# Optimization experiments

Hardware: AMD Instinct MI355X
Metric: run time of the kernel (lower is better)

Reference implementation:

```python
import jax, jax.numpy as jnp
import numpy as np

B, S, D = 2, 2048, 640
H, DH = 8, 80  # heads, dim_head
SCALE = DH ** -0.5


def setup_inputs() -> dict:
    key = jax.random.key(0)
    ks = jax.random.split(key, 7)
    std = D ** -0.5
    return {
        "x": jax.random.normal(ks[0], (B, S, D), jnp.float32),
        "encoder_hidden_states": jax.random.normal(ks[1], (B, S, D), jnp.float32),
        # Linear weights stored as [in, out] so application is x @ W
        "Wq": jax.random.normal(ks[2], (D, H * DH), jnp.float32) * std,
        "Wk": jax.random.normal(ks[3], (D, H * DH), jnp.float32) * std,
        "Wv": jax.random.normal(ks[4], (D, H * DH), jnp.float32) * std,
        "Wo": jax.random.normal(ks[5], (H * DH, D), jnp.float32) * std,
        "bo": jax.random.normal(ks[6], (D,), jnp.float32) * 0.01,
    }


def reference(x, encoder_hidden_states, Wq, Wk, Wv, Wo, bo):
    # projections (to_q/to_k/to_v have bias=False)
    q = x @ Wq                      # [B, S, H*DH]
    k = encoder_hidden_states @ Wk  # [B, S, H*DH]
    v = encoder_hidden_states @ Wv  # [B, S, H*DH]

    def split_heads(t):
        b, s, _ = t.shape
        return t.reshape(b, s, H, DH).transpose(0, 2, 1, 3)  # [B, H, S, DH]

    q, k, v = split_heads(q), split_heads(k), split_heads(v)

    # the torch loop over bh-chunks computes plain softmax attention; same math fused
    scores = jnp.einsum("bhid,bhjd->bhij", q, k) * SCALE  # [B, H, Sq, Skv]
    attn = jax.nn.softmax(scores, axis=-1)
    out = jnp.einsum("bhij,bhjd->bhid", attn, v)          # [B, H, Sq, DH]

    out = out.transpose(0, 2, 1, 3).reshape(x.shape[0], x.shape[1], H * DH)
    return out @ Wo + bo  # to_out[0]; Dropout(p=0) is identity
```

## Files before the change

### kernel.cpp

```cpp
#include <hip/hip_runtime.h>
#include <hip/hip_bf16.h>

typedef __bf16 v4bf __attribute__((ext_vector_type(4)));
typedef __bf16 v8bf __attribute__((ext_vector_type(8)));
typedef float  v4f  __attribute__((ext_vector_type(4)));

namespace {
constexpr int Bb  = 2;
constexpr int Ss  = 2048;
constexpr int Dd  = 640;
constexpr int Hh  = 8;
constexpr int DHh = 80;
constexpr int Mm  = Bb * Ss;
constexpr float kQScale = 0.11180339887498949f * 1.4426950408889634f;

__device__ __forceinline__ float4 ld4(const float* p) {
  return *reinterpret_cast<const float4*>(p);
}
}

__global__ __launch_bounds__(256)
void wtrans_kernel(const float* __restrict__ Wq, const float* __restrict__ Wk,
                   const float* __restrict__ Wv, const float* __restrict__ Wo,
                   __bf16* __restrict__ Wtq, __bf16* __restrict__ Wtk,
                   __bf16* __restrict__ Wtv, __bf16* __restrict__ Wto) {
  const int z = blockIdx.z;
  const float* W = (z == 0) ? Wq : (z == 1) ? Wk : (z == 2) ? Wv : Wo;
  __bf16* Wt = (z == 0) ? Wtq : (z == 1) ? Wtk : (z == 2) ? Wtv : Wto;
  const int k0 = blockIdx.y * 32, n0 = blockIdx.x * 32;
  __shared__ float t[32][33];
  const int tid = threadIdx.x;
  {
    int kr = tid >> 3, c4 = (tid & 7) * 4;
    float4 f = ld4(W + (size_t)(k0 + kr) * Dd + n0 + c4);
    t[kr][c4 + 0] = f.x; t[kr][c4 + 1] = f.y;
    t[kr][c4 + 2] = f.z; t[kr][c4 + 3] = f.w;
  }
  __syncthreads();
  {
    int nr = tid >> 3, kc = (tid & 7) * 4;
    v4bf p;
#pragma unroll
    for (int u = 0; u < 4; ++u) p[u] = (__bf16)t[kc + u][nr];
    *reinterpret_cast<v4bf*>(&Wt[(size_t)(n0 + nr) * Dd + k0 + kc]) = p;
  }
}

template <bool AF32>
__device__ __forceinline__ void gemm_core_db(const void* __restrict__ Ap,
                                             const __bf16* __restrict__ Bt,
                                             __bf16* As, __bf16* Bs, int m0,
                                             int n0, int rh, int ch,
                                             v4f acc[4][4]) {
  constexpr int BUF = 128 * 40;
  constexpr int NKB = Dd / 32;
  const int tid = threadIdx.x;
  const int lane = tid & 63;
  const int quad = lane >> 4, l15 = lane & 15;
  const int lr = tid >> 1;
  const int lk = (tid & 1) * 16;
  const __bf16* Bg = Bt + (size_t)(n0 + lr) * Dd + lk;
  const float* Af = (const float*)Ap;
  const __bf16* Ab = (const __bf16*)Ap;

#pragma unroll
  for (int i = 0; i < 4; ++i)
#pragma unroll
    for (int j = 0; j < 4; ++j) acc[i][j] = (v4f){0.f, 0.f, 0.f, 0.f};

  v8bf a0, a1, b0, b1;
  if constexpr (AF32) {
    const float* ap = Af + (size_t)(m0 + lr) * Dd + lk;
    float4 f0 = ld4(ap), f1 = ld4(ap + 4), f2 = ld4(ap + 8), f3 = ld4(ap + 12);
    a0[0]=(__bf16)f0.x; a0[1]=(__bf16)f0.y; a0[2]=(__bf16)f0.z; a0[3]=(__bf16)f0.w;
    a0[4]=(__bf16)f1.x; a0[5]=(__bf16)f1.y; a0[6]=(__bf16)f1.z; a0[7]=(__bf16)f1.w;
    a1[0]=(__bf16)f2.x; a1[1]=(__bf16)f2.y; a1[2]=(__bf16)f2.z; a1[3]=(__bf16)f2.w;
    a1[4]=(__bf16)f3.x; a1[5]=(__bf16)f3.y; a1[6]=(__bf16)f3.z; a1[7]=(__bf16)f3.w;
  } else {
    const __bf16* ap = Ab + (size_t)(m0 + lr) * Dd + lk;
    a0 = *reinterpret_cast<const v8bf*>(ap);
    a1 = *reinterpret_cast<const v8bf*>(ap + 8);
  }
  b0 = *reinterpret_cast<const v8bf*>(Bg);
  b1 = *reinterpret_cast<const v8bf*>(Bg + 8);
  *reinterpret_cast<v8bf*>(&As[lr * 40 + lk])     = a0;
  *reinterpret_cast<v8bf*>(&As[lr * 40 + lk + 8]) = a1;
  *reinterpret_cast<v8bf*>(&Bs[lr * 40 + lk])     = b0;
  *reinterpret_cast<v8bf*>(&Bs[lr * 40 + lk + 8]) = b1;

  for (int it = 0; it < NKB; ++it) {
    if (it + 1 < NKB) {
      const int kb = (it + 1) * 32;
      if constexpr (AF32) {
        const float* ap = Af + (size_t)(m0 + lr) * Dd + kb + lk;
        float4 f0 = ld4(ap), f1 = ld4(ap + 4), f2 = ld4(ap + 8),
               f3 = ld4(ap + 12);
        a0[0]=(__bf16)f0.x; a0[1]=(__bf16)f0.y; a0[2]=(__bf16)f0.z; a0[3]=(__bf16)f0.w;
        a0[4]=(__bf16)f1.x; a0[5]=(__bf16)f1.y; a0[6]=(__bf16)f1.z; a0[7]=(__bf16)f1.w;
        a1[0]=(__bf16)f2.x; a1[1]=(__bf16)f2.y; a1[2]=(__bf16)f2.z; a1[3]=(__bf16)f2.w;
        a1[4]=(__bf16)f3.x; a1[5]=(__bf16)f3.y; a1[6]=(__bf16)f3.z; a1[7]=(__bf16)f3.w;
      } else {
        const __bf16* ap = Ab + (size_t)(m0 + lr) * Dd + kb + lk;
        a0 = *reinterpret_cast<const v8bf*>(ap);
        a1 = *reinterpret_cast<const v8bf*>(ap + 8);
      }
      b0 = *reinterpret_cast<const v8bf*>(Bg + kb);
      b1 = *reinterpret_cast<const v8bf*>(Bg + kb + 8);
    }
    __syncthreads();
    const int cur = (it & 1) * BUF, nxt = BUF - cur;
    v8bf af[4], bv[4];
#pragma unroll
    for (int i = 0; i < 4; ++i)
      af[i] = *reinterpret_cast<const v8bf*>(
          &As[cur + (rh + i * 16 + l15) * 40 + quad * 8]);
#pragma unroll
    for (int j = 0; j < 4; ++j)
      bv[j] = *reinterpret_cast<const v8bf*>(
          &Bs[cur + (ch + j * 16 + l15) * 40 + quad * 8]);
#pragma unroll
    for (int i = 0; i < 4; ++i)
#pragma unroll
      for (int j = 0; j < 4; ++j)
        acc[i][j] = __builtin_amdgcn_mfma_f32_16x16x32_bf16(af[i], bv[j],
                                                            acc[i][j], 0, 0, 0);
    if (it + 1 < NKB) {
      *reinterpret_cast<v8bf*>(&As[nxt + lr * 40 + lk])     = a0;
      *reinterpret_cast<v8bf*>(&As[nxt + lr * 40 + lk + 8]) = a1;
      *reinterpret_cast<v8bf*>(&Bs[nxt + lr * 40 + lk])     = b0;
      *reinterpret_cast<v8bf*>(&Bs[nxt + lr * 40 + lk + 8]) = b1;
    }
  }
}

__global__ __launch_bounds__(256)
void gemm_qkv_mfma(const float* __restrict__ x, const float* __restrict__ ehs,
                   const __bf16* __restrict__ Wtq,
                   const __bf16* __restrict__ Wtk,
                   const __bf16* __restrict__ Wtv, __bf16* __restrict__ qb,
                   __bf16* __restrict__ kbuf, __bf16* __restrict__ vb) {
  const int z = blockIdx.z;
  const float* A = (z == 0) ? x : ehs;
  const __bf16* Bt = (z == 0) ? Wtq : (z == 1) ? Wtk : Wtv;
  __bf16* C = (z == 0) ? qb : (z == 1) ? kbuf : vb;
  const float scale = (z == 0) ? kQScale : 1.0f;

  __shared__ __bf16 As[2 * 128 * 40];
  __shared__ __bf16 Bs[2 * 128 * 40];
  const int tid = threadIdx.x;
  const int w = tid >> 6, lane = tid & 63;
  const int quad = lane >> 4, l15 = lane & 15;
  const int m0 = blockIdx.y * 128, n0 = blockIdx.x * 128;
  const int rh = (w >> 1) * 64, ch = (w & 1) * 64;
  v4f acc[4][4];
  gemm_core_db<true>(A, Bt, As, Bs, m0, n0, rh, ch, acc);

  if (z == 2) {
#pragma unroll
    for (int i = 0; i < 4; ++i)
#pragma unroll
      for (int j = 0; j < 4; ++j) {
        int m = m0 + rh + i * 16 + quad * 4;
        int n = n0 + ch + j * 16 + l15;
        int bb = m >> 11, tok = m & 2047;
        v4bf pk;
#pragma unroll
        for (int r = 0; r < 4; ++r) pk[r] = (__bf16)acc[i][j][r];
        *reinterpret_cast<v4bf*>(&C[((size_t)bb * Dd + n) * Ss + tok]) = pk;
      }
  } else {
#pragma unroll
    for (int i = 0; i < 4; ++i)
#pragma unroll
      for (int j = 0; j < 4; ++j) {
        int m = m0 + rh + i * 16 + quad * 4;
        int n = n0 + ch + j * 16 + l15;
#pragma unroll
        for (int r = 0; r < 4; ++r)
          C[(size_t)(m + r) * Dd + n] = (__bf16)(acc[i][j][r] * scale);
      }
  }
}

__global__ __launch_bounds__(256)
void gemm_out_mfma(const __bf16* __restrict__ A, const __bf16* __restrict__ Bt,
                   const float* __restrict__ bias, float* __restrict__ out) {
  __shared__ __bf16 As[2 * 128 * 40];
  __shared__ __bf16 Bs[2 * 128 * 40];
  const int tid = threadIdx.x;
  const int w = tid >> 6, lane = tid & 63;
  const int quad = lane >> 4, l15 = lane & 15;
  const int m0 = blockIdx.y * 128, n0 = blockIdx.x * 128;
  const int rh = (w >> 1) * 64, ch = (w & 1) * 64;
  v4f acc[4][4];
  gemm_core_db<false>(A, Bt, As, Bs, m0, n0, rh, ch, acc);

#pragma unroll
  for (int i = 0; i < 4; ++i)
#pragma unroll
    for (int j = 0; j < 4; ++j) {
      int m = m0 + rh + i * 16 + quad * 4;
      int n = n0 + ch + j * 16 + l15;
      float bn = bias[n];
#pragma unroll
      for (int r = 0; r < 4; ++r)
        out[(size_t)(m + r) * Dd + n] = acc[i][j][r] + bn;
    }
}

__global__ __launch_bounds__(256, 2)
void attn_mfma_kernel(const __bf16* __restrict__ q,
                      const __bf16* __restrict__ k,
                      const __bf16* __restrict__ vtg, __bf16* __restrict__ o) {
  constexpr int QT = 64;
  constexpr int KT = 32;
  constexpr int KW = Ss / 4;
  constexpr int NIT = KW / KT;
  constexpr int LQ = 104;
  constexpr int LV = 40;
  constexpr int KS = KT * LQ;
  constexpr int VS = 96 * LV;
  constexpr int PS = QT * LV;
  constexpr int WSZ = KS + VS + PS;
  constexpr int LM = 100;

  __shared__ __align__(16) __bf16 smem[4 * WSZ];

  const int bh = blockIdx.y;
  const int b = bh >> 3, h = bh & 7;
  const int q0 = blockIdx.x * QT;
  const int tid = threadIdx.x;
  const int w = tid >> 6;
  const int lane = tid & 63;
  const int quad = lane >> 4;
  const int l15 = lane & 15;

  __bf16* ksw = smem + w * WSZ;
  __bf16* vtw = ksw + KS;
  __bf16* psw = vtw + VS;

  const __bf16* qg  = q + (size_t)(b * Ss + q0) * Dd + h * DHh;
  const __bf16* kgb = k + (size_t)(b * Ss) * Dd + h * DHh;
  const __bf16* vgb = vtg + ((size_t)b * Dd + h * DHh) * Ss;

  v8bf qf[4][3];
#pragma unroll
  for (int qt = 0; qt < 4; ++qt)
#pragma unroll
    for (int s = 0; s < 3; ++s) {
      if (s == 2 && quad >= 2) {
        qf[qt][s] = (v8bf){};
      } else {
        qf[qt][s] = *reinterpret_cast<const v8bf*>(
            qg + (size_t)(qt * 16 + l15) * Dd + s * 32 + quad * 8);
      }
    }

  const int kgo = (lane >> 1) * Dd + (lane & 1) * 4;
  const int klo = (lane >> 1) * LQ + (lane & 1) * 4;
  const int vgo = (lane >> 3) * Ss + (lane & 7) * 4;
  const int vlo = (lane >> 3) * LV + (lane & 7) * 4;

  {
    v8bf z8 = {};
    *reinterpret_cast<v8bf*>(&ksw[(lane >> 1) * LQ + 80 + (lane & 1) * 8]) = z8;
    v8bf pad = {};
    int vr = 80 + (lane >> 2);
    if (vr == 80) {
#pragma unroll
      for (int e = 0; e < 8; ++e) pad[e] = (__bf16)1.f;
    }
    *reinterpret_cast<v8bf*>(&vtw[vr * LV + (lane & 3) * 8]) = pad;
  }
  {
    const int k0 = w * KW;
    const __bf16* kg = kgb + (size_t)k0 * Dd;
    const __bf16* vg = vgb + k0;
#pragma unroll
    for (int c = 0; c < 10; ++c) {
      *reinterpret_cast<v4bf*>(&ksw[klo + c * 8]) =
          *reinterpret_cast<const v4bf*>(kg + kgo + c * 8);
      *reinterpret_cast<v4bf*>(&vtw[vlo + c * 8 * LV]) =
          *reinterpret_cast<const v4bf*>(vg + vgo + (size_t)c * 8 * Ss);
    }
  }

  v4f Oacc[4][6];
#pragma unroll
  for (int qt = 0; qt < 4; ++qt)
#pragma unroll
    for (int mt = 0; mt < 6; ++mt) Oacc[qt][mt] = (v4f){0.f, 0.f, 0.f, 0.f};

  for (int it = 0; it < NIT; ++it) {
    const bool pf = (it + 1 < NIT);
    const int k0n = w * KW + (it + 1) * KT;
    v4bf sreg[10];
    if (pf) {
      const __bf16* kg = kgb + (size_t)k0n * Dd;
#pragma unroll
      for (int c = 0; c < 10; ++c)
        sreg[c] = *reinterpret_cast<const v4bf*>(kg + kgo + c * 8);
    }

    v4f sacc[4][2];
#pragma unroll
    for (int qt = 0; qt < 4; ++qt) {
      sacc[qt][0] = (v4f){0.f, 0.f, 0.f, 0.f};
      sacc[qt][1] = (v4f){0.f, 0.f, 0.f, 0.f};
    }
    __builtin_amdgcn_s_setprio(1);
#pragma unroll
    for (int s = 0; s < 3; ++s) {
      v8bf ak0 = *reinterpret_cast<const v8bf*>(
          &ksw[l15 * LQ + s * 32 + quad * 8]);
      v8bf ak1 = *reinterpret_cast<const v8bf*>(
          &ksw[(16 + l15) * LQ + s * 32 + quad * 8]);
#pragma unroll
      for (int qt = 0; qt < 4; ++qt) {
        sacc[qt][0] = __builtin_amdgcn_mfma_f32_16x16x32_bf16(
            ak0, qf[qt][s], sacc[qt][0], 0, 0, 0);
        sacc[qt][1] = __builtin_amdgcn_mfma_f32_16x16x32_bf16(
            ak1, qf[qt][s], sacc[qt][1], 0, 0, 0);
      }
    }
    __builtin_amdgcn_s_setprio(0);

#pragma unroll
    for (int qt = 0; qt < 4; ++qt)
#pragma unroll
      for (int mt = 0; mt < 2; ++mt) {
        v4bf pk;
#pragma unroll
        for (int r = 0; r < 4; ++r) pk[r] = (__bf16)exp2f(sacc[qt][mt][r]);
        *reinterpret_cast<v4bf*>(
            &psw[(qt * 16 + l15) * LV + mt * 16 + quad * 4]) = pk;
      }

    if (pf) {
#pragma unroll
      for (int c = 0; c < 10; ++c)
        *reinterpret_cast<v4bf*>(&ksw[klo + c * 8]) = sreg[c];
      const __bf16* vg = vgb + k0n;
#pragma unroll
      for (int c = 0; c < 10; ++c)
        sreg[c] = *reinterpret_cast<const v4bf*>(vg + vgo + (size_t)c * 8 * Ss);
    }

    v8bf bp[4];
#pragma unroll
    for (int qt = 0; qt < 4; ++qt)
      bp[qt] = *reinterpret_cast<const v8bf*>(
          &psw[(qt * 16 + l15) * LV + quad * 8]);
    __builtin_amdgcn_s_setprio(1);
#pragma unroll
    for (int mt = 0; mt < 6; ++mt) {
      v8bf av = *reinterpret_cast<const v8bf*>(
          &vtw[(mt * 16 + l15) * LV + quad * 8]);
#pragma unroll
      for (int qt = 0; qt < 4; ++qt)
        Oacc[qt][mt] = __builtin_amdgcn_mfma_f32_16x16x32_bf16(
            av, bp[qt], Oacc[qt][mt], 0, 0, 0);
    }
    __builtin_amdgcn_s_setprio(0);

    if (pf) {
#pragma unroll
      for (int c = 0; c < 10; ++c)
        *reinterpret_cast<v4bf*>(&vtw[vlo + c * 8 * LV]) = sreg[c];
    }
  }

  __syncthreads();
  float* mrg = (float*)smem;
  if (w >= 2) {
    float* base = mrg + (w - 2) * (QT * LM);
#pragma unroll
    for (int qt = 0; qt < 4; ++qt)
#pragma unroll
      for (int mt = 0; mt < 6; ++mt)
        *reinterpret_cast<v4f*>(
            &base[(qt * 16 + l15) * LM + mt * 16 + quad * 4]) = Oacc[qt][mt];
  }
  __syncthreads();
  if (w < 2) {
    const float* base = mrg + w * (QT * LM);
#pragma unroll
    for (int qt = 0; qt < 4; ++qt)
#pragma unroll
      for (int mt = 0; mt < 6; ++mt)
        Oacc[qt][mt] += *reinterpret_cast<const v4f*>(
            &base[(qt * 16 + l15) * LM + mt * 16 + quad * 4]);
  }
  __syncthreads();
  if (w == 1) {
#pragma unroll
    for (int qt = 0; qt < 4; ++qt)
#pragma unroll
      for (int mt = 0; mt < 6; ++mt)
        *reinterpret_cast<v4f*>(
            &mrg[(qt * 16 + l15) * LM + mt * 16 + quad * 4]) = Oacc[qt][mt];
  }
  __syncthreads();
  if (w == 0) {
#pragma unroll
    for (int qt = 0; qt < 4; ++qt)
#pragma unroll
      for (int mt = 0; mt < 6; ++mt)
        Oacc[qt][mt] += *reinterpret_cast<const v4f*>(
            &mrg[(qt * 16 + l15) * LM + mt * 16 + quad * 4]);
#pragma unroll
    for (int qt = 0; qt < 4; ++qt) {
      float lsum = __shfl(Oacc[qt][5][0], l15);
      float inv = 1.f / lsum;
      __bf16* og =
          o + (size_t)(b * Ss + q0 + qt * 16 + l15) * Dd + h * DHh;
#pragma unroll
      for (int mt = 0; mt < 5; ++mt) {
        v4bf pk;
#pragma unroll
        for (int r = 0; r < 4; ++r) pk[r] = (__bf16)(Oacc[qt][mt][r] * inv);
        *reinterpret_cast<v4bf*>(&og[mt * 16 + quad * 4]) = pk;
      }
    }
  }
}

extern "C" void kernel_launch(void* const* d_in, const int* in_sizes, int n_in,
                              void* d_out, int out_size, void* d_ws,
                              size_t ws_size, hipStream_t stream) {
  const float* x   = (const float*)d_in[0];
  const float* ehs = (const float*)d_in[1];
  const float* Wq  = (const float*)d_in[2];
  const float* Wk  = (const float*)d_in[3];
  const float* Wv  = (const float*)d_in[4];
  const float* Wo  = (const float*)d_in[5];
  const float* bo  = (const float*)d_in[6];
  float* out = (float*)d_out;

  __bf16* qb  = (__bf16*)d_ws;
  __bf16* kb  = qb + (size_t)Mm * Dd;
  __bf16* vb  = kb + (size_t)Mm * Dd;
  __bf16* ab  = vb + (size_t)Mm * Dd;
  __bf16* Wtq = ab + (size_t)Mm * Dd;
  __bf16* Wtk = Wtq + (size_t)Dd * Dd;
  __bf16* Wtv = Wtk + (size_t)Dd * Dd;
  __bf16* Wto = Wtv + (size_t)Dd * Dd;

  wtrans_kernel<<<dim3(Dd / 32, Dd / 32, 4), 256, 0, stream>>>(
      Wq, Wk, Wv, Wo, Wtq, Wtk, Wtv, Wto);
  gemm_qkv_mfma<<<dim3(Dd / 128, Mm / 128, 3), 256, 0, stream>>>(
      x, ehs, Wtq, Wtk, Wtv, qb, kb, vb);
  attn_mfma_kernel<<<dim3(Ss / 64, Bb * Hh), 256, 0, stream>>>(qb, kb, vb, ab);
  gemm_out_mfma<<<dim3(Dd / 128, Mm / 128), 256, 0, stream>>>(ab, Wto, bo,
                                                              out);
}
```

Before: 159.8 us.

## Software-pipeline PV MFMA one iteration behind QK and widen V loads

Restructures the attention inner loop so the P·V matrix multiply for the previous key tile runs right after the current tile's QK^T MFMAs, inside the same high-priority region, with a tail block after the loop. V is now loaded into registers per iteration using 8-element vector loads instead of 4-element ones, and stored to LDS after P is written. The aim is to overlap the exp/softmax and global-load latency with MFMA work and to cut the number of V load instructions. It keeps more live registers (vreg plus kreg), which may pressure occupancy.

```diff
diff --git a/kernel.cpp b/kernel.cpp
--- a/kernel.cpp
+++ b/kernel.cpp
@@ -258,8 +258,8 @@
 
   const int kgo = (lane >> 1) * Dd + (lane & 1) * 4;
   const int klo = (lane >> 1) * LQ + (lane & 1) * 4;
-  const int vgo = (lane >> 3) * Ss + (lane & 7) * 4;
-  const int vlo = (lane >> 3) * LV + (lane & 7) * 4;
+  const int vgo = (lane >> 2) * Ss + (lane & 3) * 8;
+  const int vlo = (lane >> 2) * LV + (lane & 3) * 8;
 
   {
     v8bf z8 = {};
@@ -273,16 +273,11 @@
     *reinterpret_cast<v8bf*>(&vtw[vr * LV + (lane & 3) * 8]) = pad;
   }
   {
-    const int k0 = w * KW;
-    const __bf16* kg = kgb + (size_t)k0 * Dd;
-    const __bf16* vg = vgb + k0;
-#pragma unroll
-    for (int c = 0; c < 10; ++c) {
+    const __bf16* kg = kgb + (size_t)(w * KW) * Dd;
+#pragma unroll
+    for (int c = 0; c < 10; ++c)
       *reinterpret_cast<v4bf*>(&ksw[klo + c * 8]) =
           *reinterpret_cast<const v4bf*>(kg + kgo + c * 8);
-      *reinterpret_cast<v4bf*>(&vtw[vlo + c * 8 * LV]) =
-          *reinterpret_cast<const v4bf*>(vg + vgo + (size_t)c * 8 * Ss);
-    }
   }
 
   v4f Oacc[4][6];
@@ -292,14 +287,13 @@
     for (int mt = 0; mt < 6; ++mt) Oacc[qt][mt] = (v4f){0.f, 0.f, 0.f, 0.f};
 
   for (int it = 0; it < NIT; ++it) {
-    const bool pf = (it + 1 < NIT);
-    const int k0n = w * KW + (it + 1) * KT;
-    v4bf sreg[10];
-    if (pf) {
-      const __bf16* kg = kgb + (size_t)k0n * Dd;
+    const bool pfK = (it + 1 < NIT);
+    v4bf kreg[10];
+    if (pfK) {
+      const __bf16* kg = kgb + (size_t)(w * KW + (it + 1) * KT) * Dd;
 #pragma unroll
       for (int c = 0; c < 10; ++c)
-        sreg[c] = *reinterpret_cast<const v4bf*>(kg + kgo + c * 8);
+        kreg[c] = *reinterpret_cast<const v4bf*>(kg + kgo + c * 8);
     }
 
     v4f sacc[4][2];
@@ -323,6 +317,32 @@
             ak1, qf[qt][s], sacc[qt][1], 0, 0, 0);
       }
     }
+
+    v8bf vreg[5];
+    {
+      const __bf16* vg = vgb + (w * KW + it * KT);
+#pragma unroll
+      for (int c = 0; c < 5; ++c)
+        vreg[c] = *reinterpret_cast<const v8bf*>(vg + vgo +
+                                                 (size_t)c * 16 * Ss);
+    }
+
+    if (it > 0) {
+      v8bf bp[4];
+#pragma unroll
+      for (int qt = 0; qt < 4; ++qt)
+        bp[qt] = *reinterpret_cast<const v8bf*>(
+            &psw[(qt * 16 + l15) * LV + quad * 8]);
+#pragma unroll
+      for (int mt = 0; mt < 6; ++mt) {
+        v8bf av = *reinterpret_cast<const v8bf*>(
+            &vtw[(mt * 16 + l15) * LV + quad * 8]);
+#pragma unroll
+        for (int qt = 0; qt < 4; ++qt)
+          Oacc[qt][mt] = __builtin_amdgcn_mfma_f32_16x16x32_bf16(
+              av, bp[qt], Oacc[qt][mt], 0, 0, 0);
+      }
+    }
     __builtin_amdgcn_s_setprio(0);
 
 #pragma unroll
@@ -336,16 +356,17 @@
             &psw[(qt * 16 + l15) * LV + mt * 16 + quad * 4]) = pk;
       }
 
-    if (pf) {
+    if (pfK) {
 #pragma unroll
       for (int c = 0; c < 10; ++c)
-        *reinterpret_cast<v4bf*>(&ksw[klo + c * 8]) = sreg[c];
-      const __bf16* vg = vgb + k0n;
-#pragma unroll
-      for (int c = 0; c < 10; ++c)
-        sreg[c] = *reinterpret_cast<const v4bf*>(vg + vgo + (size_t)c * 8 * Ss);
-    }
-
+        *reinterpret_cast<v4bf*>(&ksw[klo + c * 8]) = kreg[c];
+    }
+#pragma unroll
+    for (int c = 0; c < 5; ++c)
+      *reinterpret_cast<v8bf*>(&vtw[vlo + c * 16 * LV]) = vreg[c];
+  }
+
+  {
     v8bf bp[4];
 #pragma unroll
     for (int qt = 0; qt < 4; ++qt)
@@ -362,12 +383,6 @@
             av, bp[qt], Oacc[qt][mt], 0, 0, 0);
     }
     __builtin_amdgcn_s_setprio(0);
-
-    if (pf) {
-#pragma unroll
-      for (int c = 0; c < 10; ++c)
-        *reinterpret_cast<v4bf*>(&vtw[vlo + c * 8 * LV]) = sreg[c];
-    }
   }
 
   __syncthreads();
```

Result: no change. 156.9 us (-1.8%).
